# Optimization experiments

Measured on AMD Instinct MI355X. Metric: run time of the kernel, lower is better.

The kernel has to match this reference:

```python
import math
import jax, jax.numpy as jnp
import numpy as np

B, L, D_MODEL = 2, 2048, 768
H = 12            # num_heads == num_key_value_heads
FEAT = 16         # feature_dim
HEAD_DIM = D_MODEL // H  # 64


def taylor_exp(x):
    """Taylor-exp feature map: phi(x) = [1, x/rrd, (x (x) x)/(sqrt(2)*rd)].
    x: [..., d] -> [..., 1 + d + d^2]"""
    d = x.shape[-1]
    rd = math.sqrt(d)
    rrd = math.sqrt(rd)
    r2 = math.sqrt(2.0)
    x2 = (x[..., :, None] * x[..., None, :]).reshape(*x.shape[:-1], d * d) / r2
    ones = jnp.ones(x.shape[:-1] + (1,), dtype=x.dtype)
    return jnp.concatenate([ones, x / rrd, x2 / rd], axis=-1)


def setup_inputs() -> dict:
    key = jax.random.key(0)
    k1, k2, k3, k4, k5 = jax.random.split(key, 5)
    s = 0.02
    return {
        "hidden_states": jax.random.normal(k1, (B, L, D_MODEL), jnp.float32),
        "Wq": jax.random.normal(k2, (H * FEAT, D_MODEL), jnp.float32) * s,
        "Wk": jax.random.normal(k3, (H * FEAT, D_MODEL), jnp.float32) * s,
        "Wv": jax.random.normal(k4, (D_MODEL, D_MODEL), jnp.float32) * s,
        "Wo": jax.random.normal(k5, (D_MODEL, D_MODEL), jnp.float32) * s,
    }


def reference(hidden_states, Wq, Wk, Wv, Wo):
    b, l, d = hidden_states.shape
    # projections (torch Linear, no bias): y = x @ W.T
    q = jnp.einsum('bld,fd->blf', hidden_states, Wq).reshape(b, l, H, FEAT).transpose(0, 2, 1, 3)
    k = jnp.einsum('bld,fd->blf', hidden_states, Wk).reshape(b, l, H, FEAT).transpose(0, 2, 1, 3)
    v = jnp.einsum('bld,fd->blf', hidden_states, Wv).reshape(b, l, H, HEAD_DIM).transpose(0, 2, 1, 3)

    q = taylor_exp(q)   # [b,h,l,Dexp]
    k = taylor_exp(k)   # k_enc == k (forward clones k), v_enc == v

    # denominator: k_enc.sum over seq + causal cumsum of k
    k_state = jnp.sum(k, axis=2, keepdims=True) + jnp.cumsum(k, axis=2)  # [b,h,l,Dexp]
    z = 1.0 / jnp.sum(q * k_state, axis=-1)                              # [b,h,l]

    # quadratic scores; y1 uses causal (tril) mask, y2 uses full scores with same k,v
    A = jnp.einsum('bhnd,bhmd->bhnm', q, k)                              # [b,h,l,l]
    causal = jnp.tril(jnp.ones((l, l), dtype=A.dtype))
    A_total = A * causal + A                                             # tril(A) + A
    y = jnp.einsum('bhnm,bhme->bhne', A_total, v) * z[..., None]         # [b,h,l,e]

    out = y.transpose(0, 2, 1, 3).reshape(b, l, H * HEAD_DIM)
    return jnp.einsum('blf,df->bld', out, Wo)
```

## Files before the change

### kernel.cpp

```cpp
#include <hip/hip_runtime.h>

typedef unsigned short ushortT;
typedef __bf16 bf16x8 __attribute__((ext_vector_type(8)));
typedef float f32x4 __attribute__((ext_vector_type(4)));

#define BB   2
#define LL   2048
#define DM   768
#define HH   12
#define FT   16
#define HD   64
#define DEXP 273
#define CH   128
#define NC   16
#define NBH  24
#define NBLK 384
#define C2f  0.17677669529663687f
#define KH   768
#define KP   1536
#define SLAB_US   4096
#define SPK_BLK_US 36864
#define SPK_BLK_B  73728

__device__ __forceinline__ void split_bf16(float x, ushortT& hi, ushortT& lo) {
  unsigned b = __float_as_uint(x);
  unsigned r = b + 0x7FFFu + ((b >> 16) & 1u);
  hi = (ushortT)(r >> 16);
  float hf = __uint_as_float((unsigned)hi << 16);
  lo = (ushortT)(__float_as_uint(x - hf) >> 16);
}

__global__ __launch_bounds__(256) void pack_a(const float* __restrict__ X,
                                              ushortT* __restrict__ Xh,
                                              int total4) {
  int g = blockIdx.x * 256 + threadIdx.x;
  if (g >= total4) return;
  int m = g / 192, k4 = (g % 192) * 4;
  float4 v = *(const float4*)(X + (size_t)m * 768 + k4);
  ushortT h[4], l[4];
  split_bf16(v.x, h[0], l[0]);
  split_bf16(v.y, h[1], l[1]);
  split_bf16(v.z, h[2], l[2]);
  split_bf16(v.w, h[3], l[3]);
  ushortT* p = Xh + (size_t)m * KP + k4;
  *(ushort4*)p = *(ushort4*)h;
  *(ushort4*)(p + KH) = *(ushort4*)l;
}

__global__ __launch_bounds__(256) void pack_w(const float* __restrict__ W0,
                                              const float* __restrict__ W1,
                                              const float* __restrict__ W2,
                                              int n1, int n2,
                                              ushortT* __restrict__ Wh,
                                              int total4) {
  int g = blockIdx.x * 256 + threadIdx.x;
  if (g >= total4) return;
  int n = g / 192, k4 = (g % 192) * 4;
  const float* src = (n < n1 ? W0 + (size_t)n * 768
                    : n < n2 ? W1 + (size_t)(n - n1) * 768
                             : W2 + (size_t)(n - n2) * 768);
  float4 v = *(const float4*)(src + k4);
  ushortT h[4], l[4];
  split_bf16(v.x, h[0], l[0]);
  split_bf16(v.y, h[1], l[1]);
  split_bf16(v.z, h[2], l[2]);
  split_bf16(v.w, h[3], l[3]);
  ushortT* p = Wh + (size_t)n * KP + k4;
  *(ushort4*)p = *(ushort4*)h;
  *(ushort4*)(p + KH) = *(ushort4*)l;
}

typedef const __attribute__((address_space(1))) unsigned gq_t;
typedef __attribute__((address_space(3))) unsigned lq_t;
__device__ __forceinline__ void gload_lds16(const ushortT* g, ushortT* l) {
  __builtin_amdgcn_global_load_lds((gq_t*)g, (lq_t*)l, 16, 0, 0);
}

__global__ __launch_bounds__(256) void mfma_gemm(const ushortT* __restrict__ A,
                                                 const ushortT* __restrict__ B,
                                                 float* __restrict__ Y, int ldy,
                                                 int ntiles) {
  __shared__ ushortT sAh[128 * 32], sAl[128 * 32], sBh[64 * 32], sBl[64 * 32];
  const int blk = blockIdx.x;
  const int xcd = blk & 7, slot = blk >> 3;
  const int mtp = gridDim.x / (8 * ntiles);
  const int mt = xcd * mtp + slot / ntiles;
  const int nt = slot % ntiles;
  const int bm = mt * 128, bn = nt * 64;
  const int tid = threadIdx.x, wave = tid >> 6, lane = tid & 63;
  const int srow = lane >> 2, schk = (lane & 3) * 8;
  const ushortT* gsrc;
  ushortT* lb;
  int iters;
  switch (wave) {
    case 0:  gsrc = A + (size_t)(bm + srow) * KP + schk;      lb = sAh; iters = 8; break;
    case 1:  gsrc = A + (size_t)(bm + srow) * KP + KH + schk; lb = sAl; iters = 8; break;
    case 2:  gsrc = B + (size_t)(bn + srow) * KP + schk;      lb = sBh; iters = 4; break;
    default: gsrc = B + (size_t)(bn + srow) * KP + KH + schk; lb = sBl; iters = 4; break;
  }
  const int wm = (wave & 1) * 64, wn = (wave >> 1) * 32;
  const int fr = lane & 15, quad = lane >> 4;
  f32x4 acc[4][2] = {};
  for (int k0 = 0; k0 < KH; k0 += 32) {
    __syncthreads();
    for (int it = 0; it < iters; it++)
      gload_lds16(gsrc + k0 + (size_t)it * 16 * KP, lb + it * 512);
    __syncthreads();
    bf16x8 ah[4], al[4], bh2[2], bl2[2];
#pragma unroll
    for (int mi = 0; mi < 4; mi++) {
      ah[mi] = *(const bf16x8*)&sAh[(wm + mi * 16 + fr) * 32 + quad * 8];
      al[mi] = *(const bf16x8*)&sAl[(wm + mi * 16 + fr) * 32 + quad * 8];
    }
#pragma unroll
    for (int ni = 0; ni < 2; ni++) {
      bh2[ni] = *(const bf16x8*)&sBh[(wn + ni * 16 + fr) * 32 + quad * 8];
      bl2[ni] = *(const bf16x8*)&sBl[(wn + ni * 16 + fr) * 32 + quad * 8];
    }
#pragma unroll
    for (int mi = 0; mi < 4; mi++)
#pragma unroll
      for (int ni = 0; ni < 2; ni++) {
        acc[mi][ni] = __builtin_amdgcn_mfma_f32_16x16x32_bf16(ah[mi], bh2[ni], acc[mi][ni], 0, 0, 0);
        acc[mi][ni] = __builtin_amdgcn_mfma_f32_16x16x32_bf16(ah[mi], bl2[ni], acc[mi][ni], 0, 0, 0);
        acc[mi][ni] = __builtin_amdgcn_mfma_f32_16x16x32_bf16(al[mi], bh2[ni], acc[mi][ni], 0, 0, 0);
      }
  }
  const int orow = quad * 4;
#pragma unroll
  for (int mi = 0; mi < 4; mi++)
#pragma unroll
    for (int ni = 0; ni < 2; ni++) {
      float* yp = Y + (size_t)(bm + wm + mi * 16 + orow) * ldy + bn + wn + ni * 16 + fr;
#pragma unroll
      for (int r = 0; r < 4; r++) yp[(size_t)r * ldy] = acc[mi][ni][r];
    }
}

__global__ __launch_bounds__(256, 2) void chunk_sum_kernel(
    const float* __restrict__ qkv, ushortT* __restrict__ Spk,
    float* __restrict__ csk) {
  const int blk = blockIdx.x;
  const int bh = blk >> 4, c = blk & 15;
  const int b = bh / HH, h = bh % HH;
  __shared__ float kT[16][128];
  __shared__ ushortT phiA[288][72];
  __shared__ ushortT Vt[64][72];
  const float* base = qkv + (size_t)(b * LL + c * CH) * 1152;
  const int tid = threadIdx.x;
  const int wave = tid >> 6, lane = tid & 63;
  const int fr = lane & 15, quad = lane >> 4;
  for (int idx = tid; idx < 512; idx += 256) {
    int m = idx >> 2, i4 = (idx & 3) * 4;
    float4 k4 = *(const float4*)&base[(size_t)m * 1152 + 192 + h * 16 + i4];
    kT[i4 + 0][m] = k4.x; kT[i4 + 1][m] = k4.y;
    kT[i4 + 2][m] = k4.z; kT[i4 + 3][m] = k4.w;
  }
  const int wm2 = (wave & 1) * 144, wn2 = (wave >> 1) * 32;
  f32x4 acc[9][2] = {};
  __syncthreads();
#pragma unroll 1
  for (int s = 0; s < 4; s++) {
    const int m0 = s * 32;
    if (s) __syncthreads();
    for (int idx = tid; idx < 512; idx += 256) {
      int m = m0 + (idx >> 4), e4 = (idx & 15) * 4;
      float4 v4 = *(const float4*)&base[(size_t)m * 1152 + 384 + h * 64 + e4];
      ushortT hh[4], ll[4];
      split_bf16(v4.x, hh[0], ll[0]); split_bf16(v4.y, hh[1], ll[1]);
      split_bf16(v4.z, hh[2], ll[2]); split_bf16(v4.w, hh[3], ll[3]);
      const int mi2 = m - m0;
#pragma unroll
      for (int j = 0; j < 4; j++) {
        Vt[e4 + j][mi2] = hh[j];
        Vt[e4 + j][32 + mi2] = ll[j];
      }
    }
    for (int rr = tid; rr < 288; rr += 256) {
      const int f = rr;
      const float* pa = (f >= 17) ? kT[(f - 17) >> 4] : (f >= 1 ? kT[f - 1] : kT[0]);
      const float* pb = (f >= 17) ? kT[(f - 17) & 15] : kT[0];
      const float sc = (f == 0) ? 1.0f : (f < 17 ? 0.5f : C2f);
      const bool quadf = (f >= 17);
      const bool valid = (f < DEXP);
      ushortT hrow[32], lrow[32];
#pragma unroll
      for (int g = 0; g < 8; g++) {
        float4 a4 = *(const float4*)&pa[m0 + g * 4];
        float4 b4 = *(const float4*)&pb[m0 + g * 4];
        float v0, v1, v2, v3;
        if (f == 0) {
          v0 = v1 = v2 = v3 = 1.0f;
        } else if (!quadf) {
          v0 = sc * a4.x; v1 = sc * a4.y; v2 = sc * a4.z; v3 = sc * a4.w;
        } else {
          v0 = sc * a4.x * b4.x; v1 = sc * a4.y * b4.y;
          v2 = sc * a4.z * b4.z; v3 = sc * a4.w * b4.w;
        }
        if (!valid) { v0 = v1 = v2 = v3 = 0.0f; }
        split_bf16(v0, hrow[g * 4 + 0], lrow[g * 4 + 0]);
        split_bf16(v1, hrow[g * 4 + 1], lrow[g * 4 + 1]);
        split_bf16(v2, hrow[g * 4 + 2], lrow[g * 4 + 2]);
        split_bf16(v3, hrow[g * 4 + 3], lrow[g * 4 + 3]);
      }
      *(uint4*)&phiA[f][0] = *(uint4*)&hrow[0];
      *(uint4*)&phiA[f][8] = *(uint4*)&hrow[8];
      *(uint4*)&phiA[f][16] = *(uint4*)&hrow[16];
      *(uint4*)&phiA[f][24] = *(uint4*)&hrow[24];
      *(uint4*)&phiA[f][32] = *(uint4*)&lrow[0];
      *(uint4*)&phiA[f][40] = *(uint4*)&lrow[8];
      *(uint4*)&phiA[f][48] = *(uint4*)&lrow[16];
      *(uint4*)&phiA[f][56] = *(uint4*)&lrow[24];
    }
    __syncthreads();
    bf16x8 bhf[2], blf[2];
#pragma unroll
    for (int ni = 0; ni < 2; ni++) {
      bhf[ni] = *(const bf16x8*)&Vt[wn2 + ni * 16 + fr][quad * 8];
      blf[ni] = *(const bf16x8*)&Vt[wn2 + ni * 16 + fr][32 + quad * 8];
    }
#pragma unroll
    for (int mi = 0; mi < 9; mi++) {
      bf16x8 ah = *(const bf16x8*)&phiA[wm2 + mi * 16 + fr][quad * 8];
      bf16x8 al = *(const bf16x8*)&phiA[wm2 + mi * 16 + fr][32 + quad * 8];
#pragma unroll
      for (int ni = 0; ni < 2; ni++) {
        acc[mi][ni] = __builtin_amdgcn_mfma_f32_16x16x32_bf16(ah, bhf[ni], acc[mi][ni], 0, 0, 0);
        acc[mi][ni] = __builtin_amdgcn_mfma_f32_16x16x32_bf16(ah, blf[ni], acc[mi][ni], 0, 0, 0);
        acc[mi][ni] = __builtin_amdgcn_mfma_f32_16x16x32_bf16(al, bhf[ni], acc[mi][ni], 0, 0, 0);
      }
    }
  }
  for (int f = tid; f < DEXP; f += 256) {
    float sum = 0.0f;
    if (f == 0) {
      sum = (float)CH;
    } else if (f < 17) {
      const float* p = kT[f - 1];
      for (int m = 0; m < CH; m += 4) {
        float4 x = *(const float4*)&p[m];
        sum += x.x + x.y + x.z + x.w;
      }
      sum *= 0.5f;
    } else {
      const float* pa2 = kT[(f - 17) >> 4];
      const float* pb2 = kT[(f - 17) & 15];
      for (int m = 0; m < CH; m += 4) {
        float4 x = *(const float4*)&pa2[m];
        float4 y = *(const float4*)&pb2[m];
        sum += x.x * y.x + x.y * y.y + x.z * y.z + x.w * y.w;
      }
      sum *= C2f;
    }
    csk[(size_t)blk * DEXP + f] = sum;
  }
  __syncthreads();
  ushortT* stage = &phiA[0][0];
  ushortT* Sp = Spk + (size_t)blk * SPK_BLK_US;
#pragma unroll 1
  for (int sl = 0; sl < 9; sl++) {
    if (sl) __syncthreads();
#pragma unroll
    for (int mi = 0; mi < 9; mi++) {
      const int fb = wm2 + mi * 16;
      if ((fb >> 5) == sl) {
        const int fi0 = (fb & 31) + quad * 4;
        const int gh = fi0 >> 3;
        const int inner = (fi0 << 1) & 15;
#pragma unroll
        for (int ni = 0; ni < 2; ni++) {
          const int e = wn2 + ni * 16 + fr;
          const int es = (e & 7) << 4;
          ushortT hh2[4], ll2[4];
#pragma unroll
          for (int r = 0; r < 4; r++) split_bf16(acc[mi][ni][r], hh2[r], ll2[r]);
          char* rowp = (char*)stage + e * 128;
          *(ushort4*)(rowp + ((gh << 4) ^ es) + inner) = *(ushort4*)hh2;
          *(ushort4*)(rowp + (((gh + 4) << 4) ^ es) + inner) = *(ushort4*)ll2;
        }
      }
    }
    __syncthreads();
    uint4* gdst = (uint4*)(Sp + (size_t)sl * SLAB_US);
    const uint4* lsrc = (const uint4*)stage;
    gdst[tid] = lsrc[tid];
    gdst[tid + 256] = lsrc[tid + 256];
  }
}

__global__ __launch_bounds__(256) void prefix_kernel(ushortT* __restrict__ Spk,
                                                     float* __restrict__ csk) {
  const int gid = blockIdx.x * 256 + threadIdx.x;
  const int totS = NBH * 4608;
  if (gid < totS) {
    const int bh = gid / 4608;
    const int rem = gid % 4608;
    const int slab = rem >> 9;
    const int e = (rem >> 3) & 63;
    const int wp = rem & 7;
    const int es = (e & 7) << 4;
    const unsigned off_h = e * 128 + ((((wp >> 1)) << 4) ^ es) + ((wp & 1) << 3);
    const unsigned off_l = e * 128 + ((((wp >> 1) + 4) << 4) ^ es) + ((wp & 1) << 3);
    char* base = (char*)Spk + (size_t)bh * NC * SPK_BLK_B + slab * 8192;
    float r0[NC], r1[NC], r2[NC], r3[NC];
    float t0 = 0.f, t1 = 0.f, t2 = 0.f, t3 = 0.f;
#pragma unroll
    for (int cc = 0; cc < NC; cc++) {
      const char* p = base + (size_t)cc * SPK_BLK_B;
      ushort4 hw = *(const ushort4*)(p + off_h);
      ushort4 lw = *(const ushort4*)(p + off_l);
      r0[cc] = __uint_as_float((unsigned)hw.x << 16) + __uint_as_float((unsigned)lw.x << 16);
      r1[cc] = __uint_as_float((unsigned)hw.y << 16) + __uint_as_float((unsigned)lw.y << 16);
      r2[cc] = __uint_as_float((unsigned)hw.z << 16) + __uint_as_float((unsigned)lw.z << 16);
      r3[cc] = __uint_as_float((unsigned)hw.w << 16) + __uint_as_float((unsigned)lw.w << 16);
      t0 += r0[cc]; t1 += r1[cc]; t2 += r2[cc]; t3 += r3[cc];
    }
    float u0 = 0.f, u1 = 0.f, u2 = 0.f, u3 = 0.f;
#pragma unroll
    for (int cc = 0; cc < NC; cc++) {
      ushort4 hw, lw;
      split_bf16(u0 + t0, hw.x, lw.x);
      split_bf16(u1 + t1, hw.y, lw.y);
      split_bf16(u2 + t2, hw.z, lw.z);
      split_bf16(u3 + t3, hw.w, lw.w);
      char* p = base + (size_t)cc * SPK_BLK_B;
      *(ushort4*)(p + off_h) = hw;
      *(ushort4*)(p + off_l) = lw;
      u0 += r0[cc]; u1 += r1[cc]; u2 += r2[cc]; u3 += r3[cc];
    }
  } else {
    const int g2 = gid - totS;
    if (g2 < NBH * DEXP) {
      const int bh = g2 / DEXP;
      const int f = g2 % DEXP;
      float r[NC];
      float tot = 0.0f;
#pragma unroll
      for (int cc = 0; cc < NC; cc++) {
        r[cc] = csk[(size_t)(bh * NC + cc) * DEXP + f];
        tot += r[cc];
      }
      float run = 0.0f;
#pragma unroll
      for (int cc = 0; cc < NC; cc++) {
        csk[(size_t)(bh * NC + cc) * DEXP + f] = run + tot;
        run += r[cc];
      }
    }
  }
}

__global__ __launch_bounds__(512, 4) void fused_out(
    const float* __restrict__ qkv, const ushortT* __restrict__ Spk,
    const float* __restrict__ csk, ushortT* __restrict__ Ahat) {
  const int blk = blockIdx.x;
  const int bh = blk >> 4, c = blk & 15;
  const int b = bh / HH, h = bh % HH;
  __shared__ ushortT phiA[128][72];
  __shared__ ushortT GtD[2][4096];
  __shared__ ushortT qA1[128][24];
  __shared__ ushortT qA2[128][24];
  __shared__ ushortT kB[32][40];
  __shared__ ushortT gkS[9][64];
  __shared__ ushortT zero64[64];
  __shared__ ushortT onesRow[64];
  __shared__ float zl[128];
  const int tid = threadIdx.x;
  const int wv = tid >> 6, lane = tid & 63;
  const int fr = lane & 15, quad = lane >> 4;
  const int prow = tid >> 2, pq = tid & 3;
  const float* base = qkv + (size_t)(b * LL + c * CH) * 1152;
  const float* qrow = base + (size_t)prow * 1152 + h * 16;
  const ushortT* Gp = Spk + (size_t)blk * SPK_BLK_US;
  float qr[16];
#pragma unroll
  for (int i = 0; i < 4; i++) {
    float4 v = *(const float4*)(qrow + i * 4);
    qr[i * 4 + 0] = v.x; qr[i * 4 + 1] = v.y;
    qr[i * 4 + 2] = v.z; qr[i * 4 + 3] = v.w;
  }
  float4 vV[4];
  {
    const int mL = tid >> 4, e4 = (tid & 15) * 4;
#pragma unroll
    for (int s = 0; s < 4; s++)
      vV[s] = *(const float4*)&base[(size_t)(s * 32 + mL) * 1152 + 384 + h * 64 + e4];
  }
  float4 vK[4];
  if (tid < 128) {
    const int mL = tid >> 2, i4 = (tid & 3) * 4;
#pragma unroll
    for (int s = 0; s < 4; s++)
      vK[s] = *(const float4*)&base[(size_t)(s * 32 + mL) * 1152 + 192 + h * 16 + i4];
  }
  float gkv = 0.0f;
  if (tid < 288) {
    const float* gkp = csk + (size_t)blk * DEXP;
    gkv = (tid < DEXP) ? gkp[tid] : 0.0f;
  }
  gload_lds16(Gp + wv * 512 + lane * 8, &GtD[0][wv * 512]);
  __builtin_amdgcn_sched_barrier(0);
  {
    ushortT qh4[4], ql4[4];
#pragma unroll
    for (int i = 0; i < 4; i++) split_bf16(qr[pq * 4 + i], qh4[i], ql4[i]);
    *(ushort4*)&qA1[prow][pq * 4] = *(ushort4*)qh4;
    *(ushort4*)&qA2[prow][pq * 4] = *(ushort4*)ql4;
  }
  if (tid < 288) {
    ushortT hh, ll;
    split_bf16(gkv, hh, ll);
    gkS[tid >> 5][tid & 31] = hh;
    gkS[tid >> 5][32 + (tid & 31)] = ll;
  }
  if (tid < 64) {
    zero64[tid] = 0;
    onesRow[tid] = (tid < 32) ? (ushortT)0x3F80 : (ushortT)0;
  }
  f32x4 acc[5] = {};
#pragma unroll 1
  for (int s = 0; s < 9; s++) {
    __syncthreads();
    if (s < 8)
      gload_lds16(Gp + (s + 1) * SLAB_US + wv * 512 + lane * 8,
                  &GtD[(s + 1) & 1][wv * 512]);
    const int f0 = s * 32;
    {
      ushortT h8[8], l8[8];
#pragma unroll
      for (int j = 0; j < 8; j++) {
        const int f = f0 + pq * 8 + j;
        float v;
        if (f == 0) v = 1.0f;
        else if (f < 17) v = 0.5f * qr[f - 1];
        else if (f < DEXP) {
          const int ii = f - 17;
          v = C2f * qr[ii >> 4] * qr[ii & 15];
        } else v = 0.0f;
        split_bf16(v, h8[j], l8[j]);
      }
      *(uint4*)&phiA[prow][pq * 8] = *(uint4*)&h8[0];
      *(uint4*)&phiA[prow][32 + pq * 8] = *(uint4*)&l8[0];
    }
    bf16x8 ah = *(const bf16x8*)&phiA[wv * 16 + fr][quad * 8];
    bf16x8 al = *(const bf16x8*)&phiA[wv * 16 + fr][32 + quad * 8];
    const char* gt = (const char*)&GtD[s & 1][0];
    const int sw = (fr & 7) << 4;
#pragma unroll
    for (int ni = 0; ni < 4; ni++) {
      const int rb = (ni * 16 + fr) * 128;
      bf16x8 bh2 = *(const bf16x8*)(gt + rb + ((quad * 16) ^ sw));
      bf16x8 bl2 = *(const bf16x8*)(gt + rb + ((64 + quad * 16) ^ sw));
      acc[ni] = __builtin_amdgcn_mfma_f32_16x16x32_bf16(ah, bh2, acc[ni], 0, 0, 0);
      acc[ni] = __builtin_amdgcn_mfma_f32_16x16x32_bf16(ah, bl2, acc[ni], 0, 0, 0);
      acc[ni] = __builtin_amdgcn_mfma_f32_16x16x32_bf16(al, bh2, acc[ni], 0, 0, 0);
    }
    {
      const ushortT* gp = (fr == 0) ? &gkS[s][0] : &zero64[0];
      bf16x8 gh = *(const bf16x8*)(gp + quad * 8);
      bf16x8 gl = *(const bf16x8*)(gp + 32 + quad * 8);
      acc[4] = __builtin_amdgcn_mfma_f32_16x16x32_bf16(ah, gh, acc[4], 0, 0, 0);
      acc[4] = __builtin_amdgcn_mfma_f32_16x16x32_bf16(ah, gl, acc[4], 0, 0, 0);
      acc[4] = __builtin_amdgcn_mfma_f32_16x16x32_bf16(al, gh, acc[4], 0, 0, 0);
    }
  }
  __syncthreads();
  ushortT* VtF = &GtD[0][0];
#pragma unroll
  for (int s = 0; s < 4; s++) {
    const int m0 = s * 32;
    if (tid < 128) {
      int mL = tid >> 2, i4 = (tid & 3) * 4;
      ushortT hh[4], ll[4];
      split_bf16(vK[s].x, hh[0], ll[0]); split_bf16(vK[s].y, hh[1], ll[1]);
      split_bf16(vK[s].z, hh[2], ll[2]); split_bf16(vK[s].w, hh[3], ll[3]);
      *(ushort4*)&kB[mL][i4] = *(ushort4*)hh;
      *(ushort4*)&kB[mL][16 + i4] = *(ushort4*)ll;
    }
    {
      int mL = tid >> 4, e4 = (tid & 15) * 4;
      ushortT hh[4], ll[4];
      split_bf16(vV[s].x, hh[0], ll[0]); split_bf16(vV[s].y, hh[1], ll[1]);
      split_bf16(vV[s].z, hh[2], ll[2]); split_bf16(vV[s].w, hh[3], ll[3]);
#pragma unroll
      for (int j = 0; j < 4; j++) {
        VtF[(e4 + j) * 72 + mL] = hh[j];
        VtF[(e4 + j) * 72 + 32 + mL] = ll[j];
      }
    }
    __syncthreads();
    if (s <= (wv >> 1)) {
      bf16x8 a1 = *(const bf16x8*)&qA1[wv * 16 + fr][(quad & 1) * 8];
      bf16x8 a2 = *(const bf16x8*)&qA2[wv * 16 + fr][(quad & 1) * 8];
#pragma unroll
      for (int mtt = 0; mtt < 2; mtt++) {
        bf16x8 bk = *(const bf16x8*)&kB[mtt * 16 + fr][quad * 8];
        f32x4 sf = {};
        sf = __builtin_amdgcn_mfma_f32_16x16x32_bf16(a1, bk, sf, 0, 0, 0);
        sf = __builtin_amdgcn_mfma_f32_16x16x32_bf16(a2, bk, sf, 0, 0, 0);
        const int mg = m0 + mtt * 16 + fr;
#pragma unroll
        for (int r = 0; r < 4; r++) {
          const int rowL = wv * 16 + quad * 4 + r;
          const float sv = sf[r];
          const float p = (mg <= rowL) ? fmaf(sv, fmaf(sv, 0.03125f, 0.25f), 1.0f) : 0.0f;
          ushortT ph, pl;
          split_bf16(p, ph, pl);
          phiA[rowL][mtt * 16 + fr] = ph;
          phiA[rowL][32 + mtt * 16 + fr] = pl;
        }
      }
      bf16x8 ah = *(const bf16x8*)&phiA[wv * 16 + fr][quad * 8];
      bf16x8 al = *(const bf16x8*)&phiA[wv * 16 + fr][32 + quad * 8];
#pragma unroll
      for (int ni = 0; ni < 4; ni++) {
        bf16x8 bh2 = *(const bf16x8*)&VtF[(ni * 16 + fr) * 72 + quad * 8];
        bf16x8 bl2 = *(const bf16x8*)&VtF[(ni * 16 + fr) * 72 + 32 + quad * 8];
        acc[ni] = __builtin_amdgcn_mfma_f32_16x16x32_bf16(ah, bh2, acc[ni], 0, 0, 0);
        acc[ni] = __builtin_amdgcn_mfma_f32_16x16x32_bf16(ah, bl2, acc[ni], 0, 0, 0);
        acc[ni] = __builtin_amdgcn_mfma_f32_16x16x32_bf16(al, bh2, acc[ni], 0, 0, 0);
      }
      {
        const ushortT* op = (fr == 0) ? &onesRow[0] : &zero64[0];
        bf16x8 oh = *(const bf16x8*)(op + quad * 8);
        acc[4] = __builtin_amdgcn_mfma_f32_16x16x32_bf16(ah, oh, acc[4], 0, 0, 0);
        acc[4] = __builtin_amdgcn_mfma_f32_16x16x32_bf16(al, oh, acc[4], 0, 0, 0);
      }
    }
    __syncthreads();
  }
  if (fr == 0) {
#pragma unroll
    for (int r = 0; r < 4; r++) {
      const int rowL = wv * 16 + quad * 4 + r;
      zl[rowL] = 1.0f / acc[4][r];
    }
  }
  const size_t rowbase = (size_t)(b * LL + c * CH);
#pragma unroll
  for (int ni = 0; ni < 4; ni++)
#pragma unroll
    for (int r = 0; r < 4; r++) {
      const int rowL = wv * 16 + quad * 4 + r;
      const float val = acc[ni][r] * zl[rowL];
      ushortT hh, ll;
      split_bf16(val, hh, ll);
      ushortT* ap = Ahat + (rowbase + rowL) * (size_t)KP + h * 64 + ni * 16 + fr;
      ap[0] = hh;
      ap[KH] = ll;
    }
}

extern "C" void kernel_launch(void* const* d_in, const int* in_sizes, int n_in,
                              void* d_out, int out_size, void* d_ws, size_t ws_size,
                              hipStream_t stream) {
  const float* hs = (const float*)d_in[0];
  const float* Wq = (const float*)d_in[1];
  const float* Wk = (const float*)d_in[2];
  const float* Wv = (const float*)d_in[3];
  const float* Wo = (const float*)d_in[4];
  float* out = (float*)d_out;
  char* ws = (char*)d_ws;
  float* qkv = (float*)(ws);
  char*  attR = ws + 18874368;
  ushortT* Spk = (ushortT*)(ws + 31457280);
  float* csk = (float*)(ws + 59768832);
  ushortT* Xhat = (ushortT*)(ws + 31457280);
  ushortT* What = (ushortT*)attR;
  ushortT* Ahat = (ushortT*)attR;
  ushortT* Wohat = (ushortT*)qkv;
  const dim3 thr(256);
  pack_a<<<3072, thr, 0, stream>>>(hs, Xhat, 4096 * 192);
  pack_w<<<864, thr, 0, stream>>>(Wq, Wk, Wv, 192, 384, What, 1152 * 192);
  mfma_gemm<<<576, thr, 0, stream>>>(Xhat, What, qkv, 1152, 18);
  chunk_sum_kernel<<<NBLK, thr, 0, stream>>>(qkv, Spk, csk);
  {
    const int tot = NBH * 4608 + NBH * DEXP;
    prefix_kernel<<<(tot + 255) / 256, thr, 0, stream>>>(Spk, csk);
  }
  fused_out<<<NBLK, dim3(512), 0, stream>>>(qkv, Spk, csk, Ahat);
  pack_w<<<576, thr, 0, stream>>>(Wo, Wo, Wo, 768, 768, Wohat, 768 * 192);
  mfma_gemm<<<384, thr, 0, stream>>>(Ahat, Wohat, out, DM, 12);
}
```

Baseline: 243.0 us.

## Preload all G slabs into LDS, stage K/V once, coalesce Ahat stores

The fused_out kernel now loads all nine G slabs into LDS up front instead of double-buffering them, and converts all four K and V tiles to split-bf16 in LDS before the loops. This removes most per-iteration __syncthreads barriers. The output is staged through LDS and written with 16-byte coalesced stores instead of scattered 2-byte writes. LDS use rises to roughly 100KB, so launch bounds drop to 2 blocks per SM, lowering occupancy.

```diff
diff --git a/kernel.cpp b/kernel.cpp
--- a/kernel.cpp
+++ b/kernel.cpp
@@ -350,17 +350,18 @@
   }
 }
 
-__global__ __launch_bounds__(512, 4) void fused_out(
+__global__ __launch_bounds__(512, 2) void fused_out(
     const float* __restrict__ qkv, const ushortT* __restrict__ Spk,
     const float* __restrict__ csk, ushortT* __restrict__ Ahat) {
   const int blk = blockIdx.x;
   const int bh = blk >> 4, c = blk & 15;
   const int b = bh / HH, h = bh % HH;
+  __shared__ ushortT Gall[9][4096];
   __shared__ ushortT phiA[128][72];
-  __shared__ ushortT GtD[2][4096];
   __shared__ ushortT qA1[128][24];
   __shared__ ushortT qA2[128][24];
-  __shared__ ushortT kB[32][40];
+  __shared__ ushortT kB4[4][32][40];
+  __shared__ ushortT Vt4[4][64][72];
   __shared__ ushortT gkS[9][64];
   __shared__ ushortT zero64[64];
   __shared__ ushortT onesRow[64];
@@ -398,7 +399,9 @@
     const float* gkp = csk + (size_t)blk * DEXP;
     gkv = (tid < DEXP) ? gkp[tid] : 0.0f;
   }
-  gload_lds16(Gp + wv * 512 + lane * 8, &GtD[0][wv * 512]);
+#pragma unroll
+  for (int s = 0; s < 9; s++)
+    gload_lds16(Gp + s * SLAB_US + wv * 512 + lane * 8, &Gall[s][wv * 512]);
   __builtin_amdgcn_sched_barrier(0);
   {
     ushortT qh4[4], ql4[4];
@@ -417,13 +420,35 @@
     zero64[tid] = 0;
     onesRow[tid] = (tid < 32) ? (ushortT)0x3F80 : (ushortT)0;
   }
+  if (tid < 128) {
+    const int mL = tid >> 2, i4 = (tid & 3) * 4;
+#pragma unroll
+    for (int s = 0; s < 4; s++) {
+      ushortT hh[4], ll[4];
+      split_bf16(vK[s].x, hh[0], ll[0]); split_bf16(vK[s].y, hh[1], ll[1]);
+      split_bf16(vK[s].z, hh[2], ll[2]); split_bf16(vK[s].w, hh[3], ll[3]);
+      *(ushort4*)&kB4[s][mL][i4] = *(ushort4*)hh;
+      *(ushort4*)&kB4[s][mL][16 + i4] = *(ushort4*)ll;
+    }
+  }
+  {
+    const int mL = tid >> 4, e4 = (tid & 15) * 4;
+#pragma unroll
+    for (int s = 0; s < 4; s++) {
+      ushortT hh[4], ll[4];
+      split_bf16(vV[s].x, hh[0], ll[0]); split_bf16(vV[s].y, hh[1], ll[1]);
+      split_bf16(vV[s].z, hh[2], ll[2]); split_bf16(vV[s].w, hh[3], ll[3]);
+#pragma unroll
+      for (int j = 0; j < 4; j++) {
+        Vt4[s][e4 + j][mL] = hh[j];
+        Vt4[s][e4 + j][32 + mL] = ll[j];
+      }
+    }
+  }
   f32x4 acc[5] = {};
+  __syncthreads();
 #pragma unroll 1
   for (int s = 0; s < 9; s++) {
-    __syncthreads();
-    if (s < 8)
-      gload_lds16(Gp + (s + 1) * SLAB_US + wv * 512 + lane * 8,
-                  &GtD[(s + 1) & 1][wv * 512]);
     const int f0 = s * 32;
     {
       ushortT h8[8], l8[8];
@@ -444,7 +469,7 @@
     }
     bf16x8 ah = *(const bf16x8*)&phiA[wv * 16 + fr][quad * 8];
     bf16x8 al = *(const bf16x8*)&phiA[wv * 16 + fr][32 + quad * 8];
-    const char* gt = (const char*)&GtD[s & 1][0];
+    const char* gt = (const char*)&Gall[s][0];
     const int sw = (fr & 7) << 4;
 #pragma unroll
     for (int ni = 0; ni < 4; ni++) {
@@ -464,37 +489,15 @@
       acc[4] = __builtin_amdgcn_mfma_f32_16x16x32_bf16(al, gh, acc[4], 0, 0, 0);
     }
   }
-  __syncthreads();
-  ushortT* VtF = &GtD[0][0];
 #pragma unroll
   for (int s = 0; s < 4; s++) {
-    const int m0 = s * 32;
-    if (tid < 128) {
-      int mL = tid >> 2, i4 = (tid & 3) * 4;
-      ushortT hh[4], ll[4];
-      split_bf16(vK[s].x, hh[0], ll[0]); split_bf16(vK[s].y, hh[1], ll[1]);
-      split_bf16(vK[s].z, hh[2], ll[2]); split_bf16(vK[s].w, hh[3], ll[3]);
-      *(ushort4*)&kB[mL][i4] = *(ushort4*)hh;
-      *(ushort4*)&kB[mL][16 + i4] = *(ushort4*)ll;
-    }
-    {
-      int mL = tid >> 4, e4 = (tid & 15) * 4;
-      ushortT hh[4], ll[4];
-      split_bf16(vV[s].x, hh[0], ll[0]); split_bf16(vV[s].y, hh[1], ll[1]);
-      split_bf16(vV[s].z, hh[2], ll[2]); split_bf16(vV[s].w, hh[3], ll[3]);
-#pragma unroll
-      for (int j = 0; j < 4; j++) {
-        VtF[(e4 + j) * 72 + mL] = hh[j];
-        VtF[(e4 + j) * 72 + 32 + mL] = ll[j];
-      }
-    }
-    __syncthreads();
     if (s <= (wv >> 1)) {
+      const int m0 = s * 32;
       bf16x8 a1 = *(const bf16x8*)&qA1[wv * 16 + fr][(quad & 1) * 8];
       bf16x8 a2 = *(const bf16x8*)&qA2[wv * 16 + fr][(quad & 1) * 8];
 #pragma unroll
       for (int mtt = 0; mtt < 2; mtt++) {
-        bf16x8 bk = *(const bf16x8*)&kB[mtt * 16 + fr][quad * 8];
+        bf16x8 bk = *(const bf16x8*)&kB4[s][mtt * 16 + fr][quad * 8];
         f32x4 sf = {};
         sf = __builtin_amdgcn_mfma_f32_16x16x32_bf16(a1, bk, sf, 0, 0, 0);
         sf = __builtin_amdgcn_mfma_f32_16x16x32_bf16(a2, bk, sf, 0, 0, 0);
@@ -514,8 +517,8 @@
       bf16x8 al = *(const bf16x8*)&phiA[wv * 16 + fr][32 + quad * 8];
 #pragma unroll
       for (int ni = 0; ni < 4; ni++) {
-        bf16x8 bh2 = *(const bf16x8*)&VtF[(ni * 16 + fr) * 72 + quad * 8];
-        bf16x8 bl2 = *(const bf16x8*)&VtF[(ni * 16 + fr) * 72 + 32 + quad * 8];
+        bf16x8 bh2 = *(const bf16x8*)&Vt4[s][ni * 16 + fr][quad * 8];
+        bf16x8 bl2 = *(const bf16x8*)&Vt4[s][ni * 16 + fr][32 + quad * 8];
         acc[ni] = __builtin_amdgcn_mfma_f32_16x16x32_bf16(ah, bh2, acc[ni], 0, 0, 0);
         acc[ni] = __builtin_amdgcn_mfma_f32_16x16x32_bf16(ah, bl2, acc[ni], 0, 0, 0);
         acc[ni] = __builtin_amdgcn_mfma_f32_16x16x32_bf16(al, bh2, acc[ni], 0, 0, 0);
@@ -527,7 +530,6 @@
         acc[4] = __builtin_amdgcn_mfma_f32_16x16x32_bf16(al, oh, acc[4], 0, 0, 0);
       }
     }
-    __syncthreads();
   }
   if (fr == 0) {
 #pragma unroll
@@ -536,7 +538,8 @@
       zl[rowL] = 1.0f / acc[4][r];
     }
   }
-  const size_t rowbase = (size_t)(b * LL + c * CH);
+  __syncthreads();
+  ushortT* ost = &Gall[0][0];
 #pragma unroll
   for (int ni = 0; ni < 4; ni++)
 #pragma unroll
@@ -545,10 +548,21 @@
       const float val = acc[ni][r] * zl[rowL];
       ushortT hh, ll;
       split_bf16(val, hh, ll);
-      ushortT* ap = Ahat + (rowbase + rowL) * (size_t)KP + h * 64 + ni * 16 + fr;
-      ap[0] = hh;
-      ap[KH] = ll;
-    }
+      ost[rowL * 136 + ni * 16 + fr] = hh;
+      ost[rowL * 136 + 64 + ni * 16 + fr] = ll;
+    }
+  __syncthreads();
+  const size_t rowbase = (size_t)(b * LL + c * CH);
+#pragma unroll
+  for (int j = 0; j < 4; j++) {
+    const int seg = tid + j * 512;
+    const int row = seg >> 4;
+    const int half = (seg >> 3) & 1;
+    const int off = (seg & 7) * 8;
+    uint4 v = *(const uint4*)&ost[row * 136 + half * 64 + off];
+    ushortT* ap = Ahat + (rowbase + row) * (size_t)KP + half * KH + h * 64 + off;
+    *(uint4*)ap = v;
+  }
 }
 
 extern "C" void kernel_launch(void* const* d_in, const int* in_sizes, int n_in,
```

After: 259.8 us. 6.9% more time.
